# Kernel tuning notes

Hardware: AMD Instinct MI355X
Metric: run time of the kernel (lower is better)

Reference implementation:

```python
import jax, jax.numpy as jnp
import numpy as np

DIM = 1024
HEADS = 16
HEAD_DIM = DIM // HEADS
N = 4096
EPS = 1e-5


def setup_inputs() -> dict:
    key = jax.random.key(0)
    ks = jax.random.split(key, 12)
    s = DIM ** -0.5  # init scale for weights
    return {
        "z1": jax.random.normal(ks[0], (N, DIM), jnp.float32),
        "z2": jax.random.normal(ks[1], (N, DIM), jnp.float32),
        "wq": jax.random.normal(ks[2], (DIM, DIM), jnp.float32) * s,
        "bq": jax.random.normal(ks[3], (DIM,), jnp.float32) * 0.01,
        "wk": jax.random.normal(ks[4], (DIM, DIM), jnp.float32) * s,
        "bk": jax.random.normal(ks[5], (DIM,), jnp.float32) * 0.01,
        "wv1": jax.random.normal(ks[6], (DIM, DIM), jnp.float32) * s,
        "bv1": jax.random.normal(ks[7], (DIM,), jnp.float32) * 0.01,
        "wv2": jax.random.normal(ks[8], (DIM, DIM), jnp.float32) * s,
        "bv2": jax.random.normal(ks[9], (DIM,), jnp.float32) * 0.01,
        "g1": jnp.ones((DIM,), jnp.float32),
        "be1": jnp.zeros((DIM,), jnp.float32),
        "g2": jnp.ones((DIM,), jnp.float32),
        "be2": jnp.zeros((DIM,), jnp.float32),
    }


def _layernorm(x, g, b):
    mu = jnp.mean(x, axis=-1, keepdims=True)
    var = jnp.mean(jnp.square(x - mu), axis=-1, keepdims=True)
    return (x - mu) * jax.lax.rsqrt(var + EPS) * g + b


def _split_heads(x):  # [n, dim] -> [h, n, c]
    n = x.shape[0]
    return x.reshape(n, HEADS, HEAD_DIM).swapaxes(0, 1)


def reference(z1, z2, wq, bq, wk, bk, wv1, bv1, wv2, bv2, g1, be1, g2, be2):
    scale = DIM ** -0.5
    n1 = _layernorm(z1, g1, be1)
    n2 = _layernorm(z2, g2, be2)
    q = _split_heads(n1 @ wq.T + bq)    # [h, n, c]
    k = _split_heads(n2 @ wk.T + bk)    # [h, m, c]
    v = _split_heads(n2 @ wv1.T + bv1)  # [h, m, c]
    v1 = _split_heads(n1 @ wv2.T + bv2) # [h, n, c]
    sim = jnp.einsum('hnc,hmc->hnm', q, k) * scale
    attn = jax.nn.softmax(sim, axis=-1)                       # [h, n, m]
    z_c = jnp.einsum('hnm,hmc->hnc', attn, v)                 # attn @ v
    c_z = jnp.einsum('hnm,hnc->hmc', attn, v1)                # attn.T @ v1
    z_c = z_c.swapaxes(0, 1).reshape(z1.shape[0], DIM)
    c_z = c_z.swapaxes(0, 1).reshape(z2.shape[0], DIM)
    # torch's attn.squeeze(0) is a no-op for HEADS > 1
    return z_c, c_z, attn
```

## Files before the change

### kernel.cpp

```cpp
#include <hip/hip_runtime.h>

#define NN 4096
#define DIM 1024
#define HEADS 16
#define HD 64
#define SCALE 0.03125f
#define EXP2S 0.04508422002778011f

typedef __attribute__((ext_vector_type(8))) short bf16x8;
typedef __attribute__((ext_vector_type(4))) short short4v;
typedef __attribute__((ext_vector_type(4))) float f32x4;
typedef __attribute__((ext_vector_type(4))) unsigned int u32x4;

__device__ __forceinline__ short f2bf(float f) {
  unsigned int x = __float_as_uint(f);
  unsigned int r = x + 0x7FFFu + ((x >> 16) & 1u);
  return (short)(r >> 16);
}
__device__ __forceinline__ float bf2f(short s) {
  return __uint_as_float(((unsigned int)(unsigned short)s) << 16);
}
__device__ __forceinline__ unsigned int cvtpk(float a, float b) {
  unsigned int r;
  asm("v_cvt_pk_bf16_f32 %0, %1, %2" : "=v"(r) : "v"(a), "v"(b));
  return r;
}
__device__ __forceinline__ float exp2x(float x) {
  float r;
  asm("v_exp_f32 %0, %1" : "=v"(r) : "v"(x));
  return r;
}

#define GLL16(gp, lp) __builtin_amdgcn_global_load_lds( \
    (const __attribute__((address_space(1))) unsigned int*)(gp), \
    (__attribute__((address_space(3))) unsigned int*)(lp), 16, 0, 0)

#define MFMA16(a, b, c) __builtin_amdgcn_mfma_f32_16x16x32_bf16(a, b, c, 0, 0, 0)

__global__ __launch_bounds__(256) void ln_kernel(
    const float* __restrict__ z1, const float* __restrict__ z2,
    const float* __restrict__ g1, const float* __restrict__ be1,
    const float* __restrict__ g2, const float* __restrict__ be2,
    short* __restrict__ n1, short* __restrict__ n2) {
  int row = blockIdx.x;
  int which = blockIdx.y;
  const float* src = (which ? z2 : z1) + (size_t)row * DIM;
  const float* g  = which ? g2 : g1;
  const float* be = which ? be2 : be1;
  short* dst = (which ? n2 : n1) + (size_t)row * DIM;
  int t = threadIdx.x;
  float4 v = ((const float4*)src)[t];
  float s  = v.x + v.y + v.z + v.w;
  float s2 = v.x*v.x + v.y*v.y + v.z*v.z + v.w*v.w;
#pragma unroll
  for (int off = 32; off >= 1; off >>= 1) {
    s  += __shfl_xor(s, off);
    s2 += __shfl_xor(s2, off);
  }
  __shared__ __align__(16) float ls[8];
  int wid = t >> 6;
  if ((t & 63) == 0) { ls[wid] = s; ls[wid + 4] = s2; }
  __syncthreads();
  s  = ls[0] + ls[1] + ls[2] + ls[3];
  s2 = ls[4] + ls[5] + ls[6] + ls[7];
  float mu = s * (1.0f / DIM);
  float var = s2 * (1.0f / DIM) - mu * mu;
  float rs = rsqrtf(var + 1e-5f);
  float4 gv = ((const float4*)g)[t];
  float4 bv = ((const float4*)be)[t];
  short4v o;
  o.x = f2bf((v.x - mu) * rs * gv.x + bv.x);
  o.y = f2bf((v.y - mu) * rs * gv.y + bv.y);
  o.z = f2bf((v.z - mu) * rs * gv.z + bv.z);
  o.w = f2bf((v.w - mu) * rs * gv.w + bv.w);
  ((short4v*)dst)[t] = o;
}

__global__ __launch_bounds__(256) void cvt_w_kernel(
    const float* __restrict__ w0, const float* __restrict__ w1,
    const float* __restrict__ w2, const float* __restrict__ w3,
    short* __restrict__ wb) {
  int y = blockIdx.y;
  const float* src = (y == 0) ? w0 : (y == 1) ? w1 : (y == 2) ? w2 : w3;
  size_t i = (size_t)blockIdx.x * 256 + threadIdx.x;
  float4 v = ((const float4*)src)[i];
  short4v o;
  o.x = f2bf(v.x); o.y = f2bf(v.y); o.z = f2bf(v.z); o.w = f2bf(v.w);
  ((short4v*)(wb + (size_t)y * DIM * DIM))[i] = o;
}

__global__ __launch_bounds__(256) void proj_kernel(
    const short* __restrict__ n1, const short* __restrict__ n2,
    const short* __restrict__ wb,
    const float* __restrict__ bq, const float* __restrict__ bk,
    const float* __restrict__ bv1, const float* __restrict__ bv2,
    short* __restrict__ q, short* __restrict__ k,
    short* __restrict__ vT, short* __restrict__ v1T) {
  int z = blockIdx.z;
  const short* A = (z == 1 || z == 2) ? n2 : n1;
  const short* B = wb + (size_t)z * DIM * DIM;
  const float* bias = (z == 0) ? bq : (z == 1) ? bk : (z == 2) ? bv1 : bv2;
  int i0 = blockIdx.y * 128, j0 = blockIdx.x * 128;
  __shared__ __align__(16) short As[128 * 32];
  __shared__ __align__(16) short Bs[128 * 32];
  int t = threadIdx.x;
  int wid = t >> 6, lane = t & 63, g = lane >> 4, l15 = lane & 15;
  int wi = (wid >> 1) * 64, wj = (wid & 1) * 64;
  f32x4 acc[4][4] = {};
  for (int kt = 0; kt < DIM; kt += 32) {
    __syncthreads();
#pragma unroll
    for (int e = 0; e < 2; ++e) {
      int lin = e * 256 + t;
      int row = lin >> 2, kc = (lin & 3) * 8;
      GLL16(A + (size_t)(i0 + row) * DIM + kt + kc, As + lin * 8);
      GLL16(B + (size_t)(j0 + row) * DIM + kt + kc, Bs + lin * 8);
    }
    __syncthreads();
    bf16x8 af[4], bfr[4];
#pragma unroll
    for (int it = 0; it < 4; ++it)
      af[it] = *(const bf16x8*)(As + (wi + it * 16 + l15) * 32 + g * 8);
#pragma unroll
    for (int jt = 0; jt < 4; ++jt)
      bfr[jt] = *(const bf16x8*)(Bs + (wj + jt * 16 + l15) * 32 + g * 8);
#pragma unroll
    for (int it = 0; it < 4; ++it)
#pragma unroll
      for (int jt = 0; jt < 4; ++jt)
        acc[it][jt] = MFMA16(af[it], bfr[jt], acc[it][jt]);
  }
  if (z < 2) {
    short* out = (z == 0) ? q : k;
#pragma unroll
    for (int jt = 0; jt < 4; ++jt) {
      int j = j0 + wj + jt * 16 + l15;
      float bj = bias[j];
#pragma unroll
      for (int it = 0; it < 4; ++it) {
        int i = i0 + wi + it * 16 + g * 4;
#pragma unroll
        for (int r = 0; r < 4; ++r)
          out[(size_t)(i + r) * DIM + j] = f2bf(acc[it][jt][r] + bj);
      }
    }
  } else {
    short* out = (z == 2) ? vT : v1T;
#pragma unroll
    for (int jt = 0; jt < 4; ++jt) {
      int j = j0 + wj + jt * 16 + l15;
      float bj = bias[j];
#pragma unroll
      for (int it = 0; it < 4; ++it) {
        int i = i0 + wi + it * 16 + g * 4;
        short4v o;
#pragma unroll
        for (int r = 0; r < 4; ++r) o[r] = f2bf(acc[it][jt][r] + bj);
        *(short4v*)(out + (size_t)j * NN + i) = o;
      }
    }
  }
}

__global__ __launch_bounds__(256, 4) void p2zc_kernel(
    const short* __restrict__ q, const short* __restrict__ k,
    const short* __restrict__ vT, float* __restrict__ attn,
    float* __restrict__ zc, float* __restrict__ iSx) {
  int bid = (int)(blockIdx.y * gridDim.x + blockIdx.x);
  int vid = (bid & 7) * 128 + (bid >> 3);
  int h = vid >> 6;
  int nblk = vid & 63;
  int t = threadIdx.x, wid = t >> 6, lane = t & 63;
  int g = lane >> 4, l15 = lane & 15;
  int nw = nblk * 64 + wid * 16;

  const short* qp = q + (size_t)(nw + l15) * DIM + h * HD + g * 8;
  bf16x8 qb0 = *(const bf16x8*)(qp);
  bf16x8 qb1 = *(const bf16x8*)(qp + 32);

  __shared__ __align__(16) short Ks[128 * 64];
  __shared__ __align__(16) short Vs[64 * 128];
  const short* kb = k + h * HD;
  const short* vb = vT + (size_t)h * HD * NN;

  f32x4 Sp = {0.f, 0.f, 0.f, 0.f};
  for (int mc = 0; mc < NN; mc += 128) {
    __syncthreads();
#pragma unroll
    for (int e = 0; e < 4; ++e) {
      int L = e * 256 + t, row = L >> 3, c = L & 7;
      GLL16(kb + (size_t)(mc + row) * DIM + ((c ^ (row & 7)) * 8), Ks + L * 8);
    }
    __syncthreads();
#pragma unroll
    for (int mt = 0; mt < 8; ++mt) {
      const short* kr = Ks + (mt * 16 + l15) * 64;
      bf16x8 ka0 = *(const bf16x8*)(kr + ((g ^ (l15 & 7)) * 8));
      bf16x8 ka1 = *(const bf16x8*)(kr + (((g + 4) ^ (l15 & 7)) * 8));
      f32x4 acc = {0.f, 0.f, 0.f, 0.f};
      acc = MFMA16(ka0, qb0, acc);
      acc = MFMA16(ka1, qb1, acc);
#pragma unroll
      for (int r = 0; r < 4; ++r) Sp[r] += exp2x(acc[r] * EXP2S);
    }
  }
  float S = Sp[0] + Sp[1] + Sp[2] + Sp[3];
  S += __shfl_xor(S, 16);
  S += __shfl_xor(S, 32);
  float iS = 1.0f / S;
  if (lane < 16) iSx[h * NN + nw + l15] = iS;

  float* ab = attn + (size_t)h * NN * NN;
  f32x4 azc[4] = {};
  for (int mc = 0; mc < NN; mc += 128) {
    __syncthreads();
#pragma unroll
    for (int e = 0; e < 4; ++e) {
      int L = e * 256 + t, row = L >> 3, c = L & 7;
      GLL16(kb + (size_t)(mc + row) * DIM + ((c ^ (row & 7)) * 8), Ks + L * 8);
    }
#pragma unroll
    for (int e = 0; e < 4; ++e) {
      int L = e * 256 + t, row = L >> 4, c = L & 15;
      GLL16(vb + (size_t)row * NN + mc + ((c ^ (row & 15)) * 8), Vs + L * 8);
    }
    __syncthreads();
    float p[8][4];
#pragma unroll
    for (int mt = 0; mt < 8; ++mt) {
      const short* kr = Ks + (mt * 16 + l15) * 64;
      bf16x8 ka0 = *(const bf16x8*)(kr + ((g ^ (l15 & 7)) * 8));
      bf16x8 ka1 = *(const bf16x8*)(kr + (((g + 4) ^ (l15 & 7)) * 8));
      f32x4 acc = {0.f, 0.f, 0.f, 0.f};
      acc = MFMA16(ka0, qb0, acc);
      acc = MFMA16(ka1, qb1, acc);
      f32x4 pv;
#pragma unroll
      for (int r = 0; r < 4; ++r) { pv[r] = exp2x(acc[r] * EXP2S) * iS; p[mt][r] = pv[r]; }
      *(f32x4*)(ab + (size_t)(nw + l15) * NN + mc + mt * 16 + g * 4) = pv;
    }
#pragma unroll
    for (int km = 0; km < 4; ++km) {
      unsigned int a0p = cvtpk(p[2*km][0],   p[2*km][1]);
      unsigned int a1p = cvtpk(p[2*km][2],   p[2*km][3]);
      unsigned int b0p = cvtpk(p[2*km+1][0], p[2*km+1][1]);
      unsigned int b1p = cvtpk(p[2*km+1][2], p[2*km+1][3]);
      int s0 = ((g & 1) * 2) * 16 + l15, s1 = s0 + 16;
      bool hi = g >= 2;
      unsigned int w0a = __shfl(a0p, s0), w0b = __shfl(b0p, s0);
      unsigned int w1a = __shfl(a1p, s0), w1b = __shfl(b1p, s0);
      unsigned int w2a = __shfl(a0p, s1), w2b = __shfl(b0p, s1);
      unsigned int w3a = __shfl(a1p, s1), w3b = __shfl(b1p, s1);
      union { u32x4 u; bf16x8 s; } pw;
      pw.u[0] = hi ? w0b : w0a; pw.u[1] = hi ? w1b : w1a;
      pw.u[2] = hi ? w2b : w2a; pw.u[3] = hi ? w3b : w3a;
#pragma unroll
      for (int ct = 0; ct < 4; ++ct) {
        bf16x8 pb = *(const bf16x8*)(Vs + (ct * 16 + l15) * 128 + (((km * 4 + g) ^ l15) * 8));
        azc[ct] = MFMA16(pw.s, pb, azc[ct]);
      }
    }
  }
#pragma unroll
  for (int ct = 0; ct < 4; ++ct)
#pragma unroll
    for (int r = 0; r < 4; ++r)
      zc[(size_t)(nw + g * 4 + r) * DIM + h * HD + ct * 16 + l15] = azc[ct][r];
}

__global__ __launch_bounds__(256) void v1scale_kernel(
    short* __restrict__ v1T, const float* __restrict__ iSx) {
  int row = blockIdx.y;
  int h = row >> 6;
  int n0 = (int)(blockIdx.x * 2048) + threadIdx.x * 8;
  short* p = v1T + (size_t)row * NN + n0;
  bf16x8 v = *(const bf16x8*)p;
  const float* isb = iSx + h * NN + n0;
  f32x4 i0 = ((const f32x4*)isb)[0];
  f32x4 i1 = ((const f32x4*)isb)[1];
  union { u32x4 u; bf16x8 s; } o;
  o.u[0] = cvtpk(bf2f(v[0]) * i0[0], bf2f(v[1]) * i0[1]);
  o.u[1] = cvtpk(bf2f(v[2]) * i0[2], bf2f(v[3]) * i0[3]);
  o.u[2] = cvtpk(bf2f(v[4]) * i1[0], bf2f(v[5]) * i1[1]);
  o.u[3] = cvtpk(bf2f(v[6]) * i1[2], bf2f(v[7]) * i1[3]);
  *(bf16x8*)p = o.s;
}

__global__ __launch_bounds__(256, 4) void czr_kernel(
    const short* __restrict__ q, const short* __restrict__ k,
    const short* __restrict__ v1T, float* __restrict__ cz) {
  int bid = (int)(blockIdx.y * gridDim.x + blockIdx.x);
  int vid = (bid & 7) * 128 + (bid >> 3);
  int h = vid >> 6;
  int mblk = vid & 63;
  int t = threadIdx.x, wid = t >> 6, lane = t & 63;
  int g = lane >> 4, l15 = lane & 15;
  int mw = mblk * 64 + wid * 16;

  const short* kp = k + (size_t)(mw + l15) * DIM + h * HD + g * 8;
  bf16x8 kb0 = *(const bf16x8*)(kp);
  bf16x8 kb1 = *(const bf16x8*)(kp + 32);

  __shared__ __align__(16) short Qs[128 * 64];
  __shared__ __align__(16) short V1s[64 * 128];
  const short* qb = q + h * HD;
  const short* vb = v1T + (size_t)h * HD * NN;

  f32x4 acz[4] = {};
  for (int nc = 0; nc < NN; nc += 128) {
    __syncthreads();
#pragma unroll
    for (int e = 0; e < 4; ++e) {
      int L = e * 256 + t, row = L >> 3, c = L & 7;
      GLL16(qb + (size_t)(nc + row) * DIM + ((c ^ (row & 7)) * 8), Qs + L * 8);
    }
#pragma unroll
    for (int e = 0; e < 4; ++e) {
      int L = e * 256 + t, row = L >> 4, c = L & 15;
      GLL16(vb + (size_t)row * NN + nc + ((c ^ (row & 15)) * 8), V1s + L * 8);
    }
    __syncthreads();
    float p[8][4];
#pragma unroll
    for (int nt = 0; nt < 8; ++nt) {
      const short* qr = Qs + (nt * 16 + l15) * 64;
      bf16x8 qa0 = *(const bf16x8*)(qr + ((g ^ (l15 & 7)) * 8));
      bf16x8 qa1 = *(const bf16x8*)(qr + (((g + 4) ^ (l15 & 7)) * 8));
      f32x4 acc = {0.f, 0.f, 0.f, 0.f};
      acc = MFMA16(qa0, kb0, acc);
      acc = MFMA16(qa1, kb1, acc);
#pragma unroll
      for (int r = 0; r < 4; ++r) p[nt][r] = exp2x(acc[r] * EXP2S);
    }
#pragma unroll
    for (int kn = 0; kn < 4; ++kn) {
      unsigned int a0p = cvtpk(p[2*kn][0],   p[2*kn][1]);
      unsigned int a1p = cvtpk(p[2*kn][2],   p[2*kn][3]);
      unsigned int b0p = cvtpk(p[2*kn+1][0], p[2*kn+1][1]);
      unsigned int b1p = cvtpk(p[2*kn+1][2], p[2*kn+1][3]);
      int s0 = ((g & 1) * 2) * 16 + l15, s1 = s0 + 16;
      bool hi = g >= 2;
      unsigned int w0a = __shfl(a0p, s0), w0b = __shfl(b0p, s0);
      unsigned int w1a = __shfl(a1p, s0), w1b = __shfl(b1p, s0);
      unsigned int w2a = __shfl(a0p, s1), w2b = __shfl(b0p, s1);
      unsigned int w3a = __shfl(a1p, s1), w3b = __shfl(b1p, s1);
      union { u32x4 u; bf16x8 s; } pw;
      pw.u[0] = hi ? w0b : w0a; pw.u[1] = hi ? w1b : w1a;
      pw.u[2] = hi ? w2b : w2a; pw.u[3] = hi ? w3b : w3a;
#pragma unroll
      for (int ct = 0; ct < 4; ++ct) {
        bf16x8 pb = *(const bf16x8*)(V1s + (ct * 16 + l15) * 128 + (((kn * 4 + g) ^ l15) * 8));
        acz[ct] = MFMA16(pw.s, pb, acz[ct]);
      }
    }
  }
#pragma unroll
  for (int ct = 0; ct < 4; ++ct)
#pragma unroll
    for (int r = 0; r < 4; ++r)
      cz[(size_t)(mw + g * 4 + r) * DIM + h * HD + ct * 16 + l15] = acz[ct][r];
}

extern "C" void kernel_launch(void* const* d_in, const int* in_sizes, int n_in,
                              void* d_out, int out_size, void* d_ws, size_t ws_size,
                              hipStream_t stream) {
  static const int expect[14] = {4194304, 4194304, 1048576, 1024, 1048576, 1024,
                                 1048576, 1024, 1048576, 1024, 1024, 1024, 1024, 1024};
  if (n_in != 14) return;
  for (int i = 0; i < 14; ++i) if (in_sizes[i] != expect[i]) return;
  if (out_size != 2 * NN * DIM + (size_t)HEADS * NN * NN) return;

  const float* z1  = (const float*)d_in[0];
  const float* z2  = (const float*)d_in[1];
  const float* wq  = (const float*)d_in[2];
  const float* bq  = (const float*)d_in[3];
  const float* wk  = (const float*)d_in[4];
  const float* bk  = (const float*)d_in[5];
  const float* wv1 = (const float*)d_in[6];
  const float* bv1 = (const float*)d_in[7];
  const float* wv2 = (const float*)d_in[8];
  const float* bv2 = (const float*)d_in[9];
  const float* g1  = (const float*)d_in[10];
  const float* be1 = (const float*)d_in[11];
  const float* g2  = (const float*)d_in[12];
  const float* be2 = (const float*)d_in[13];

  float* out  = (float*)d_out;
  float* zc   = out;
  float* cz   = out + (size_t)NN * DIM;
  float* attn = out + 2 * (size_t)NN * DIM;

  short* n1 = (short*)zc;
  short* n2 = (short*)cz;
  short* wb = (short*)attn;

  char* ws = (char*)d_ws;
  const size_t MB = 1024 * 1024;
  short* q   = (short*)(ws);
  short* k   = (short*)(ws + 8 * MB);
  short* vT  = (short*)(ws + 16 * MB);
  short* v1T = (short*)(ws + 24 * MB);
  float* iSx = (float*)(ws + 32 * MB);

  ln_kernel<<<dim3(NN, 2), 256, 0, stream>>>(z1, z2, g1, be1, g2, be2, n1, n2);
  cvt_w_kernel<<<dim3(DIM * DIM / 1024, 4), 256, 0, stream>>>(wq, wk, wv1, wv2, wb);
  proj_kernel<<<dim3(DIM / 128, NN / 128, 4), 256, 0, stream>>>(n1, n2, wb, bq, bk, bv1, bv2, q, k, vT, v1T);
  p2zc_kernel<<<dim3(NN / 64, HEADS), 256, 0, stream>>>(q, k, vT, attn, zc, iSx);
  v1scale_kernel<<<dim3(NN / 2048, DIM), 256, 0, stream>>>(v1T, iSx);
  czr_kernel<<<dim3(NN / 64, HEADS), 256, 0, stream>>>(q, k, v1T, cz);
}
```

Before: 535.2 us.

## Split softmax row-sum pass into its own kernel with 128-row tiles and fused v1 scaling

Moves the first pass, which computes the softmax denominators, out of p2zc into a separate sums_kernel. Each block handles 128 query rows, so every K tile loaded into shared memory is reused across twice as many rows. The same kernel also applies the 1/S scaling to v1T, which removes the standalone v1scale launch. p2zc now just reads the precomputed iS. The trade-off is fewer blocks in the sum pass and a changed occupancy pattern.

After: 578.4 us. 8.1% more time.

```diff
diff --git a/kernel.cpp b/kernel.cpp
--- a/kernel.cpp
+++ b/kernel.cpp
@@ -162,10 +162,86 @@
   }
 }
 
+__global__ __launch_bounds__(256, 4) void sums_kernel(
+    const short* __restrict__ q, const short* __restrict__ k,
+    short* __restrict__ v1T, float* __restrict__ iSx) {
+  int bid = (int)(blockIdx.y * gridDim.x + blockIdx.x);
+  int vid = (bid & 7) * 64 + (bid >> 3);
+  int h = vid >> 5;
+  int base = (vid & 31) * 128;
+  int t = threadIdx.x, wid = t >> 6, lane = t & 63;
+  int g = lane >> 4, l15 = lane & 15;
+  int nw[2] = {base + wid * 16, base + 64 + wid * 16};
+
+  bf16x8 qb[2][2];
+#pragma unroll
+  for (int tl = 0; tl < 2; ++tl) {
+    const short* qp = q + (size_t)(nw[tl] + l15) * DIM + h * HD + g * 8;
+    qb[tl][0] = *(const bf16x8*)(qp);
+    qb[tl][1] = *(const bf16x8*)(qp + 32);
+  }
+
+  __shared__ __align__(16) short Ks[128 * 64];
+  __shared__ float ls[128];
+  const short* kb = k + h * HD;
+
+  float Sp[2][4] = {};
+  for (int mc = 0; mc < NN; mc += 128) {
+    __syncthreads();
+#pragma unroll
+    for (int e = 0; e < 4; ++e) {
+      int L = e * 256 + t, row = L >> 3, c = L & 7;
+      GLL16(kb + (size_t)(mc + row) * DIM + ((c ^ (row & 7)) * 8), Ks + L * 8);
+    }
+    __syncthreads();
+#pragma unroll
+    for (int mt = 0; mt < 8; ++mt) {
+      const short* kr = Ks + (mt * 16 + l15) * 64;
+      bf16x8 ka0 = *(const bf16x8*)(kr + ((g ^ (l15 & 7)) * 8));
+      bf16x8 ka1 = *(const bf16x8*)(kr + (((g + 4) ^ (l15 & 7)) * 8));
+#pragma unroll
+      for (int tl = 0; tl < 2; ++tl) {
+        f32x4 acc = {0.f, 0.f, 0.f, 0.f};
+        acc = MFMA16(ka0, qb[tl][0], acc);
+        acc = MFMA16(ka1, qb[tl][1], acc);
+#pragma unroll
+        for (int r = 0; r < 4; ++r) Sp[tl][r] += exp2x(acc[r] * EXP2S);
+      }
+    }
+  }
+  __syncthreads();
+#pragma unroll
+  for (int tl = 0; tl < 2; ++tl) {
+    float S = Sp[tl][0] + Sp[tl][1] + Sp[tl][2] + Sp[tl][3];
+    S += __shfl_xor(S, 16);
+    S += __shfl_xor(S, 32);
+    float iS = 1.0f / S;
+    if (lane < 16) {
+      iSx[h * NN + nw[tl] + l15] = iS;
+      ls[nw[tl] - base + l15] = iS;
+    }
+  }
+  __syncthreads();
+#pragma unroll
+  for (int e = 0; e < 4; ++e) {
+    int id = e * 256 + t;
+    int c = id >> 4, ch = id & 15;
+    short* p = v1T + (size_t)(h * HD + c) * NN + base + ch * 8;
+    bf16x8 v = *(const bf16x8*)p;
+    const float* isp = ls + ch * 8;
+    union { u32x4 u; bf16x8 s; } o;
+    o.u[0] = cvtpk(bf2f(v[0]) * isp[0], bf2f(v[1]) * isp[1]);
+    o.u[1] = cvtpk(bf2f(v[2]) * isp[2], bf2f(v[3]) * isp[3]);
+    o.u[2] = cvtpk(bf2f(v[4]) * isp[4], bf2f(v[5]) * isp[5]);
+    o.u[3] = cvtpk(bf2f(v[6]) * isp[6], bf2f(v[7]) * isp[7]);
+    *(bf16x8*)p = o.s;
+  }
+}
+
 __global__ __launch_bounds__(256, 4) void p2zc_kernel(
     const short* __restrict__ q, const short* __restrict__ k,
-    const short* __restrict__ vT, float* __restrict__ attn,
-    float* __restrict__ zc, float* __restrict__ iSx) {
+    const short* __restrict__ vT, const float* __restrict__ iSx,
+    float* __restrict__ attn, float* __restrict__ zc) {
   int bid = (int)(blockIdx.y * gridDim.x + blockIdx.x);
   int vid = (bid & 7) * 128 + (bid >> 3);
   int h = vid >> 6;
@@ -177,38 +253,12 @@
   const short* qp = q + (size_t)(nw + l15) * DIM + h * HD + g * 8;
   bf16x8 qb0 = *(const bf16x8*)(qp);
   bf16x8 qb1 = *(const bf16x8*)(qp + 32);
+  float iS = iSx[h * NN + nw + l15];
 
   __shared__ __align__(16) short Ks[128 * 64];
   __shared__ __align__(16) short Vs[64 * 128];
   const short* kb = k + h * HD;
   const short* vb = vT + (size_t)h * HD * NN;
-
-  f32x4 Sp = {0.f, 0.f, 0.f, 0.f};
-  for (int mc = 0; mc < NN; mc += 128) {
-    __syncthreads();
-#pragma unroll
-    for (int e = 0; e < 4; ++e) {
-      int L = e * 256 + t, row = L >> 3, c = L & 7;
-      GLL16(kb + (size_t)(mc + row) * DIM + ((c ^ (row & 7)) * 8), Ks + L * 8);
-    }
-    __syncthreads();
-#pragma unroll
-    for (int mt = 0; mt < 8; ++mt) {
-      const short* kr = Ks + (mt * 16 + l15) * 64;
-      bf16x8 ka0 = *(const bf16x8*)(kr + ((g ^ (l15 & 7)) * 8));
-      bf16x8 ka1 = *(const bf16x8*)(kr + (((g + 4) ^ (l15 & 7)) * 8));
-      f32x4 acc = {0.f, 0.f, 0.f, 0.f};
-      acc = MFMA16(ka0, qb0, acc);
-      acc = MFMA16(ka1, qb1, acc);
-#pragma unroll
-      for (int r = 0; r < 4; ++r) Sp[r] += exp2x(acc[r] * EXP2S);
-    }
-  }
-  float S = Sp[0] + Sp[1] + Sp[2] + Sp[3];
-  S += __shfl_xor(S, 16);
-  S += __shfl_xor(S, 32);
-  float iS = 1.0f / S;
-  if (lane < 16) iSx[h * NN + nw + l15] = iS;
 
   float* ab = attn + (size_t)h * NN * NN;
   f32x4 azc[4] = {};
@@ -268,24 +318,6 @@
       zc[(size_t)(nw + g * 4 + r) * DIM + h * HD + ct * 16 + l15] = azc[ct][r];
 }
 
-__global__ __launch_bounds__(256) void v1scale_kernel(
-    short* __restrict__ v1T, const float* __restrict__ iSx) {
-  int row = blockIdx.y;
-  int h = row >> 6;
-  int n0 = (int)(blockIdx.x * 2048) + threadIdx.x * 8;
-  short* p = v1T + (size_t)row * NN + n0;
-  bf16x8 v = *(const bf16x8*)p;
-  const float* isb = iSx + h * NN + n0;
-  f32x4 i0 = ((const f32x4*)isb)[0];
-  f32x4 i1 = ((const f32x4*)isb)[1];
-  union { u32x4 u; bf16x8 s; } o;
-  o.u[0] = cvtpk(bf2f(v[0]) * i0[0], bf2f(v[1]) * i0[1]);
-  o.u[1] = cvtpk(bf2f(v[2]) * i0[2], bf2f(v[3]) * i0[3]);
-  o.u[2] = cvtpk(bf2f(v[4]) * i1[0], bf2f(v[5]) * i1[1]);
-  o.u[3] = cvtpk(bf2f(v[6]) * i1[2], bf2f(v[7]) * i1[3]);
-  *(bf16x8*)p = o.s;
-}
-
 __global__ __launch_bounds__(256, 4) void czr_kernel(
     const short* __restrict__ q, const short* __restrict__ k,
     const short* __restrict__ v1T, float* __restrict__ cz) {
@@ -405,7 +437,7 @@
   ln_kernel<<<dim3(NN, 2), 256, 0, stream>>>(z1, z2, g1, be1, g2, be2, n1, n2);
   cvt_w_kernel<<<dim3(DIM * DIM / 1024, 4), 256, 0, stream>>>(wq, wk, wv1, wv2, wb);
   proj_kernel<<<dim3(DIM / 128, NN / 128, 4), 256, 0, stream>>>(n1, n2, wb, bq, bk, bv1, bv2, q, k, vT, v1T);
-  p2zc_kernel<<<dim3(NN / 64, HEADS), 256, 0, stream>>>(q, k, vT, attn, zc, iSx);
-  v1scale_kernel<<<dim3(NN / 2048, DIM), 256, 0, stream>>>(v1T, iSx);
+  sums_kernel<<<dim3(NN / 128, HEADS), 256, 0, stream>>>(q, k, v1T, iSx);
+  p2zc_kernel<<<dim3(NN / 64, HEADS), 256, 0, stream>>>(q, k, vT, iSx, attn, zc);
   czr_kernel<<<dim3(NN / 64, HEADS), 256, 0, stream>>>(q, k, v1T, cz);
 }
```
